# Performance work log

Measured on AMD Instinct MI355X. Metric: run time of the kernel, lower is better.

The kernel has to match this reference:

```python
import jax, jax.numpy as jnp
import numpy as np

B = 65536
IN = 64
H = 128
OUT = 2


def setup_inputs() -> dict:
    key = jax.random.key(0)
    ks = jax.random.split(key, 16)
    s_in = 1.0 / np.sqrt(IN)
    s_h = 1.0 / np.sqrt(H)
    d = {}
    d["x"] = jax.random.normal(ks[0], (B, IN), dtype=jnp.float32)
    # initial state (module resets to zeros per day)
    d["h0"] = jnp.zeros((H,), dtype=jnp.float32)
    d["c0"] = jnp.zeros((B, H), dtype=jnp.float32)
    # input->hidden linears (with bias), torch Linear layout [out, in]
    for i, name in enumerate(["f", "i", "o", "c"]):
        d[f"Wx{name}"] = jax.random.uniform(ks[1 + i], (H, IN), jnp.float32, -s_in, s_in)
        d[f"bx{name}"] = jax.random.uniform(ks[5 + i], (H,), jnp.float32, -s_in, s_in)
        d[f"Wh{name}"] = jax.random.uniform(ks[9 + i], (H, H), jnp.float32, -s_h, s_h)
    d["Wy"] = jax.random.uniform(ks[13], (OUT, H), jnp.float32, -s_h, s_h)
    d["by"] = jax.random.uniform(ks[14], (OUT,), jnp.float32, -s_h, s_h)
    return d


def reference(x, h0, c0, Wxf, bxf, Wxi, bxi, Wxo, bxo, Wxc, bxc, Whf, Whi, Who, Whc, Wy, by):
    # hidden recurrent contributions (h0 is a length-H vector, broadcast over batch)
    hi = h0 @ Whi.T  # [H]
    hf = h0 @ Whf.T
    ho = h0 @ Who.T
    hc = h0 @ Whc.T
    i = jax.nn.sigmoid(x @ Wxi.T + bxi + hi)  # [B, H]
    f = jax.nn.sigmoid(x @ Wxf.T + bxf + hf)
    o = jax.nn.sigmoid(x @ Wxo.T + bxo + ho)
    c_til = jnp.tanh(x @ Wxc.T + bxc + hc)
    c = f * c0 + i * c_til
    h = o * jnp.tanh(c)
    y_hat = h @ Wy.T + by  # [B, OUT]
    return y_hat
```

## Files before the change

kernel.cpp:

```cpp
#include <hip/hip_runtime.h>


#define B_SIZE 65536

typedef __bf16 bf16x8 __attribute__((ext_vector_type(8)));
typedef __bf16 bf16x4 __attribute__((ext_vector_type(4)));
typedef float f32x4 __attribute__((ext_vector_type(4)));

__device__ __forceinline__ float fsig(float x) {
    float e = __builtin_amdgcn_exp2f(-1.442695040888963f * x);
    return __builtin_amdgcn_rcpf(1.0f + e);
}
__device__ __forceinline__ float ftanh(float x) {
    float e = __builtin_amdgcn_exp2f(2.885390081777927f * x);
    return 1.0f - 2.0f * __builtin_amdgcn_rcpf(e + 1.0f);
}

__global__ void bias_kernel(const float* __restrict__ h0,
                            const float* __restrict__ Whf, const float* __restrict__ Whi,
                            const float* __restrict__ Who, const float* __restrict__ Whc,
                            const float* __restrict__ bxf, const float* __restrict__ bxi,
                            const float* __restrict__ bxo, const float* __restrict__ bxc,
                            float* __restrict__ bias512) {
    int j = blockIdx.x * 64 + threadIdx.x;
    int g = j >> 7, r = j & 127;
    const float* Wh = (g == 0) ? Whf : (g == 1) ? Whi : (g == 2) ? Who : Whc;
    const float* bx = (g == 0) ? bxf : (g == 1) ? bxi : (g == 2) ? bxo : bxc;
    float s = bx[r];
    const float* row = Wh + r * 128;
#pragma unroll 8
    for (int k = 0; k < 128; ++k) s += h0[k] * row[k];
    bias512[j] = s;
}

__launch_bounds__(256, 2)
__global__ void lstm_kernel(const float* __restrict__ x, const float* __restrict__ c0,
                            const float* __restrict__ Wxf, const float* __restrict__ Wxi,
                            const float* __restrict__ Wxo, const float* __restrict__ Wxc,
                            const float* __restrict__ Wy, const float* __restrict__ by,
                            const float* __restrict__ bias512, float* __restrict__ out) {
    __shared__ __bf16 xs[1024];
    __shared__ float yred[4][16][2];

    const int tid  = threadIdx.x;
    const int lane = tid & 63;
    const int w    = tid >> 6;
    const int q    = lane >> 4;
    const int n15  = lane & 15;

    const float* Wxg[4] = {Wxf, Wxi, Wxo, Wxc};
    bf16x8 bw[4][2][2];
    float biasv[4][2];
#pragma unroll
    for (int g = 0; g < 4; ++g) {
#pragma unroll
        for (int cb = 0; cb < 2; ++cb) {
            const int n = w * 32 + cb * 16 + n15;
            biasv[g][cb] = bias512[g * 128 + n];
#pragma unroll
            for (int kb = 0; kb < 2; ++kb) {
                const float* p = Wxg[g] + n * 64 + kb * 32 + q * 8;
                float4 lo = *(const float4*)p;
                float4 hi = *(const float4*)(p + 4);
                bf16x8 v;
                v[0] = (__bf16)lo.x; v[1] = (__bf16)lo.y; v[2] = (__bf16)lo.z; v[3] = (__bf16)lo.w;
                v[4] = (__bf16)hi.x; v[5] = (__bf16)hi.y; v[6] = (__bf16)hi.z; v[7] = (__bf16)hi.w;
                bw[g][cb][kb] = v;
            }
        }
    }
    float wyv[2][2];
#pragma unroll
    for (int o = 0; o < 2; ++o)
#pragma unroll
        for (int cb = 0; cb < 2; ++cb)
            wyv[o][cb] = Wy[o * 128 + w * 32 + cb * 16 + n15];
    const float by0 = by[0], by1 = by[1];

    constexpr int ITERS = (B_SIZE / 16) / 512;
    const int tile0 = blockIdx.x * ITERS;

    const int xrow = tid >> 4;
    const int k4   = (tid & 15) * 4;
    const int sidx = (k4 >> 5) * 512 + ((k4 & 31) >> 3) * 128 + xrow * 8 + (k4 & 7);

    float4 xr = *(const float4*)(x + (size_t)(tile0 * 16 + xrow) * 64 + k4);
    {
        bf16x4 v; v[0] = (__bf16)xr.x; v[1] = (__bf16)xr.y; v[2] = (__bf16)xr.z; v[3] = (__bf16)xr.w;
        *(bf16x4*)&xs[sidx] = v;
    }
    __syncthreads();

    for (int it = 0; it < ITERS; ++it) {
        const int tile = tile0 + it;
        const int b0 = tile * 16;

        bf16x8 a0 = *(const bf16x8*)&xs[lane * 8];
        bf16x8 a1 = *(const bf16x8*)&xs[512 + lane * 8];

        const int tn = (it + 1 < ITERS) ? (tile + 1) : tile;
        xr = *(const float4*)(x + (size_t)(tn * 16 + xrow) * 64 + k4);

        float c0v[2][4];
#pragma unroll
        for (int cb = 0; cb < 2; ++cb)
#pragma unroll
            for (int r = 0; r < 4; ++r)
                c0v[cb][r] = c0[(size_t)(b0 + q * 4 + r) * 128 + w * 32 + cb * 16 + n15];

        f32x4 acc[4][2];
#pragma unroll
        for (int g = 0; g < 4; ++g)
#pragma unroll
            for (int cb = 0; cb < 2; ++cb) {
                float b = biasv[g][cb];
                f32x4 t = {b, b, b, b};
                acc[g][cb] = t;
            }
#pragma unroll
        for (int g = 0; g < 4; ++g)
#pragma unroll
            for (int cb = 0; cb < 2; ++cb) {
                acc[g][cb] = __builtin_amdgcn_mfma_f32_16x16x32_bf16(a0, bw[g][cb][0], acc[g][cb], 0, 0, 0);
                acc[g][cb] = __builtin_amdgcn_mfma_f32_16x16x32_bf16(a1, bw[g][cb][1], acc[g][cb], 0, 0, 0);
            }

        float p0[4] = {0.f, 0.f, 0.f, 0.f};
        float p1[4] = {0.f, 0.f, 0.f, 0.f};
#pragma unroll
        for (int cb = 0; cb < 2; ++cb)
#pragma unroll
            for (int r = 0; r < 4; ++r) {
                float fg = fsig(acc[0][cb][r]);
                float ig = fsig(acc[1][cb][r]);
                float og = fsig(acc[2][cb][r]);
                float ct = ftanh(acc[3][cb][r]);
                float c  = fg * c0v[cb][r] + ig * ct;
                float h  = og * ftanh(c);
                p0[r] += h * wyv[0][cb];
                p1[r] += h * wyv[1][cb];
            }
#pragma unroll
        for (int m = 1; m < 16; m <<= 1) {
#pragma unroll
            for (int r = 0; r < 4; ++r) {
                p0[r] += __shfl_xor(p0[r], m, 64);
                p1[r] += __shfl_xor(p1[r], m, 64);
            }
        }
        if (n15 == 0) {
#pragma unroll
            for (int r = 0; r < 4; ++r) {
                yred[w][q * 4 + r][0] = p0[r];
                yred[w][q * 4 + r][1] = p1[r];
            }
        }
        __syncthreads();
        if (tid < 32) {
            int row = tid >> 1, o = tid & 1;
            float s = (o ? by1 : by0) + yred[0][row][o] + yred[1][row][o] +
                      yred[2][row][o] + yred[3][row][o];
            out[(size_t)(b0 + row) * 2 + o] = s;
        }
        {
            bf16x4 v; v[0] = (__bf16)xr.x; v[1] = (__bf16)xr.y; v[2] = (__bf16)xr.z; v[3] = (__bf16)xr.w;
            *(bf16x4*)&xs[sidx] = v;
        }
        __syncthreads();
    }
}

extern "C" void kernel_launch(void* const* d_in, const int* in_sizes, int n_in,
                              void* d_out, int out_size, void* d_ws, size_t ws_size,
                              hipStream_t stream) {
    const float* x   = (const float*)d_in[0];
    const float* h0  = (const float*)d_in[1];
    const float* c0  = (const float*)d_in[2];
    const float* Wxf = (const float*)d_in[3];
    const float* bxf = (const float*)d_in[4];
    const float* Whf = (const float*)d_in[5];
    const float* Wxi = (const float*)d_in[6];
    const float* bxi = (const float*)d_in[7];
    const float* Whi = (const float*)d_in[8];
    const float* Wxo = (const float*)d_in[9];
    const float* bxo = (const float*)d_in[10];
    const float* Who = (const float*)d_in[11];
    const float* Wxc = (const float*)d_in[12];
    const float* bxc = (const float*)d_in[13];
    const float* Whc = (const float*)d_in[14];
    const float* Wy  = (const float*)d_in[15];
    const float* by  = (const float*)d_in[16];
    float* out = (float*)d_out;
    float* bias512 = (float*)d_ws;

    bias_kernel<<<8, 64, 0, stream>>>(h0, Whf, Whi, Who, Whc, bxf, bxi, bxo, bxc, bias512);
    lstm_kernel<<<512, 256, 0, stream>>>(x, c0, Wxf, Wxi, Wxo, Wxc, Wy, by, bias512, out);
}
```

Before: 133.8 us.

## Double-buffer x tile and y-reduction in LDS to drop one barrier per iteration

The shared x tile and y partial-sum buffers become ping-pong buffers, so the next tile's x is written to the other buffer before a single barrier and the second __syncthreads per iteration goes away. The loads of x and c0 and the output store now use nontemporal hints, and the c0 loads are issued before the LDS reads. The bias kernel's dot product is vectorised with float4 loads. The aim is less barrier stalling and less cache pollution from streaming data, at the cost of twice the LDS footprint and a cross-iteration buffer-reuse invariant that relies on the single barrier.

```diff
diff --git a/kernel.cpp b/kernel.cpp
--- a/kernel.cpp
+++ b/kernel.cpp
@@ -26,10 +26,14 @@
     int g = j >> 7, r = j & 127;
     const float* Wh = (g == 0) ? Whf : (g == 1) ? Whi : (g == 2) ? Who : Whc;
     const float* bx = (g == 0) ? bxf : (g == 1) ? bxi : (g == 2) ? bxo : bxc;
+    const f32x4* row4 = (const f32x4*)(Wh + r * 128);
+    const f32x4* h04  = (const f32x4*)h0;
     float s = bx[r];
-    const float* row = Wh + r * 128;
-#pragma unroll 8
-    for (int k = 0; k < 128; ++k) s += h0[k] * row[k];
+#pragma unroll
+    for (int k = 0; k < 32; ++k) {
+        f32x4 a = row4[k], b = h04[k];
+        s += a.x * b.x + a.y * b.y + a.z * b.z + a.w * b.w;
+    }
     bias512[j] = s;
 }
 
@@ -39,8 +43,8 @@
                             const float* __restrict__ Wxo, const float* __restrict__ Wxc,
                             const float* __restrict__ Wy, const float* __restrict__ by,
                             const float* __restrict__ bias512, float* __restrict__ out) {
-    __shared__ __bf16 xs[1024];
-    __shared__ float yred[4][16][2];
+    __shared__ __bf16 xs[2][1024];
+    __shared__ float yred[2][4][16][2];
 
     const int tid  = threadIdx.x;
     const int lane = tid & 63;
@@ -60,8 +64,8 @@
 #pragma unroll
             for (int kb = 0; kb < 2; ++kb) {
                 const float* p = Wxg[g] + n * 64 + kb * 32 + q * 8;
-                float4 lo = *(const float4*)p;
-                float4 hi = *(const float4*)(p + 4);
+                f32x4 lo = *(const f32x4*)p;
+                f32x4 hi = *(const f32x4*)(p + 4);
                 bf16x8 v;
                 v[0] = (__bf16)lo.x; v[1] = (__bf16)lo.y; v[2] = (__bf16)lo.z; v[3] = (__bf16)lo.w;
                 v[4] = (__bf16)hi.x; v[5] = (__bf16)hi.y; v[6] = (__bf16)hi.z; v[7] = (__bf16)hi.w;
@@ -84,29 +88,33 @@
     const int k4   = (tid & 15) * 4;
     const int sidx = (k4 >> 5) * 512 + ((k4 & 31) >> 3) * 128 + xrow * 8 + (k4 & 7);
 
-    float4 xr = *(const float4*)(x + (size_t)(tile0 * 16 + xrow) * 64 + k4);
+    f32x4 xr = __builtin_nontemporal_load(
+        (const f32x4*)(x + (size_t)(tile0 * 16 + xrow) * 64 + k4));
     {
         bf16x4 v; v[0] = (__bf16)xr.x; v[1] = (__bf16)xr.y; v[2] = (__bf16)xr.z; v[3] = (__bf16)xr.w;
-        *(bf16x4*)&xs[sidx] = v;
+        *(bf16x4*)&xs[0][sidx] = v;
     }
     __syncthreads();
 
     for (int it = 0; it < ITERS; ++it) {
+        const int p = it & 1;
         const int tile = tile0 + it;
         const int b0 = tile * 16;
 
-        bf16x8 a0 = *(const bf16x8*)&xs[lane * 8];
-        bf16x8 a1 = *(const bf16x8*)&xs[512 + lane * 8];
+        float c0v[2][4];
+        const float* c0p = c0 + (size_t)(b0 + q * 4) * 128 + w * 32 + n15;
+#pragma unroll
+        for (int cb = 0; cb < 2; ++cb)
+#pragma unroll
+            for (int r = 0; r < 4; ++r)
+                c0v[cb][r] = __builtin_nontemporal_load(c0p + r * 128 + cb * 16);
+
+        bf16x8 a0 = *(const bf16x8*)&xs[p][lane * 8];
+        bf16x8 a1 = *(const bf16x8*)&xs[p][512 + lane * 8];
 
         const int tn = (it + 1 < ITERS) ? (tile + 1) : tile;
-        xr = *(const float4*)(x + (size_t)(tn * 16 + xrow) * 64 + k4);
-
-        float c0v[2][4];
-#pragma unroll
-        for (int cb = 0; cb < 2; ++cb)
-#pragma unroll
-            for (int r = 0; r < 4; ++r)
-                c0v[cb][r] = c0[(size_t)(b0 + q * 4 + r) * 128 + w * 32 + cb * 16 + n15];
+        xr = __builtin_nontemporal_load(
+            (const f32x4*)(x + (size_t)(tn * 16 + xrow) * 64 + k4));
 
         f32x4 acc[4][2];
 #pragma unroll
@@ -151,22 +159,21 @@
         if (n15 == 0) {
 #pragma unroll
             for (int r = 0; r < 4; ++r) {
-                yred[w][q * 4 + r][0] = p0[r];
-                yred[w][q * 4 + r][1] = p1[r];
-            }
+                yred[p][w][q * 4 + r][0] = p0[r];
+                yred[p][w][q * 4 + r][1] = p1[r];
+            }
+        }
+        {
+            bf16x4 v; v[0] = (__bf16)xr.x; v[1] = (__bf16)xr.y; v[2] = (__bf16)xr.z; v[3] = (__bf16)xr.w;
+            *(bf16x4*)&xs[p ^ 1][sidx] = v;
         }
         __syncthreads();
         if (tid < 32) {
             int row = tid >> 1, o = tid & 1;
-            float s = (o ? by1 : by0) + yred[0][row][o] + yred[1][row][o] +
-                      yred[2][row][o] + yred[3][row][o];
-            out[(size_t)(b0 + row) * 2 + o] = s;
-        }
-        {
-            bf16x4 v; v[0] = (__bf16)xr.x; v[1] = (__bf16)xr.y; v[2] = (__bf16)xr.z; v[3] = (__bf16)xr.w;
-            *(bf16x4*)&xs[sidx] = v;
-        }
-        __syncthreads();
+            float s = (o ? by1 : by0) + yred[p][0][row][o] + yred[p][1][row][o] +
+                      yred[p][2][row][o] + yred[p][3][row][o];
+            __builtin_nontemporal_store(s, out + (size_t)(b0 + row) * 2 + o);
+        }
     }
 }
 
```

Result: no change. 134.8 us (+0.7%).
